# Performance work log

Hardware: AMD Instinct MI355X
Metric: run time of the kernel (lower is better)

The kernel has to match this reference:

```python
import math
import jax, jax.numpy as jnp
import numpy as np

N_HEAD = 16
N_CLUSTER = 64
GROUP_SIZE = 256


def _sinusoidal(n, d):
    # emb[p, 2j] = sin(p*div_j), emb[p, 2j+1] = cos(p*div_j)  (interleaved, as in torch source)
    pos = jnp.arange(n, dtype=jnp.float32)[:, None]
    div = jnp.exp(jnp.arange(0, d, 2, dtype=jnp.float32) * (-math.log(10000.0) / d))
    ang = pos * div  # [n, d//2]
    return jnp.stack([jnp.sin(ang), jnp.cos(ang)], axis=-1).reshape(n, d)


def _rotary(pe, x):
    # Faithful to source: sin = first half of interleaved table, cos = second half,
    # and the function RETURNS ONLY the rotated term (not x*cos + rot*sin).
    d = x.shape[-1]
    sin, cos = pe[..., : d // 2], pe[..., d // 2 :]
    x_even, x_odd = x[..., ::2], x[..., 1::2]
    out = jnp.stack([-x_odd * cos, x_even * sin], axis=-1)
    return out.reshape(jnp.broadcast_shapes(x.shape[:-1] + (d // 2,), out.shape[:-1]) + (2,)).reshape(x.shape) if False else jnp.broadcast_to(out, x.shape[:-1] + (d // 2, 2)).reshape(x.shape)


def _forward(x, w_attn, b_attn, w_proj, b_proj, w_assign):
    B, T, C = x.shape
    H, nc, gs = N_HEAD, N_CLUSTER, GROUP_SIZE
    hd = C // H
    ntpc = T // nc                 # tokens per cluster
    G = T // gs                    # number of groups
    ncpg = gs // ntpc              # clusters summarized per group
    c_max = (G - 1) * ncpg         # max cluster-KV length (padded)

    qkv = x @ w_attn.T + b_attn    # [B, T, 3C]
    q, k, v = jnp.split(qkv, 3, axis=-1)

    # ---- soft cluster summarization (block-diagonal softmax over each cluster's tokens) ----
    x_r = x.reshape(B, nc, ntpc, C)
    logits = jnp.einsum('bctd,cd->bct', x_r, w_assign)        # only diagonal cluster survives the mask
    w = jax.nn.softmax(logits, axis=-1)                        # [B, nc, ntpc]
    ck = jnp.einsum('bct,bctd->bcd', w, k.reshape(B, nc, ntpc, C))  # [B, nc, C]
    cv = jnp.einsum('bct,bctd->bcd', w, v.reshape(B, nc, ntpc, C))

    # ---- split into groups & heads ----
    qg = q.reshape(B, G, gs, H, hd).transpose(0, 1, 3, 2, 4)   # [B,G,H,gs,hd]
    kl = k.reshape(B, G, gs, H, hd).transpose(0, 1, 3, 2, 4)
    vl = v.reshape(B, G, gs, H, hd).transpose(0, 1, 3, 2, 4)
    kc = ck[:, :c_max].reshape(B, c_max, H, hd)                # [B,c_max,H,hd]
    vc = cv[:, :c_max].reshape(B, c_max, H, hd)

    # ---- rotary (positions restart per group; cluster tokens occupy positions 0..c-1) ----
    S = _sinusoidal(c_max + gs, hd)
    qr = _rotary(S[:gs], qg)                                   # q positions 0..gs-1 in every group
    kcr = _rotary(S[:c_max, None, :], kc)                      # cluster slot j -> position j
    pos_local = jnp.arange(G)[:, None] * ncpg + jnp.arange(gs)[None, :]  # [G,gs]
    klr = _rotary(S[pos_local][None, :, None], kl)             # local key p in group g -> pos g*ncpg+p

    # ---- attention: cluster KV (fully visible, masked to first g*ncpg) + local causal ----
    scale = 1.0 / math.sqrt(hd)
    sc = jnp.einsum('bghqd,bchd->bghqc', qr, kcr) * scale      # [B,G,H,gs,c_max]
    sl = jnp.einsum('bghqd,bghkd->bghqk', qr, klr) * scale     # [B,G,H,gs,gs]
    cmask = jnp.arange(c_max)[None, :] < (jnp.arange(G) * ncpg)[:, None]  # [G,c_max]
    sc = jnp.where(cmask[None, :, None, None, :], sc, -jnp.inf)
    lmask = jnp.tril(jnp.ones((gs, gs), dtype=bool))
    sl = jnp.where(lmask, sl, -jnp.inf)
    p = jax.nn.softmax(jnp.concatenate([sc, sl], axis=-1), axis=-1)
    pc, pl = p[..., :c_max], p[..., c_max:]
    y = jnp.einsum('bghqc,bchd->bghqd', pc, vc) + jnp.einsum('bghqk,bghkd->bghqd', pl, vl)
    y = y.transpose(0, 1, 3, 2, 4).reshape(B, T, C)
    return y @ w_proj.T + b_proj


def setup_inputs() -> dict:
    key = jax.random.key(0)
    ks = jax.random.split(key, 4)
    B, T, C, NC = 4, 4096, 1024, N_CLUSTER
    x = jax.random.normal(ks[0], (B, T, C), jnp.float32)
    w_attn = jax.random.normal(ks[1], (3 * C, C), jnp.float32) * 0.02
    b_attn = jnp.zeros((3 * C,), jnp.float32)
    w_proj = jax.random.normal(ks[2], (C, C), jnp.float32) * 0.02
    b_proj = jnp.zeros((C,), jnp.float32)
    w_assign = jax.random.normal(ks[3], (NC, C), jnp.float32) * 0.02
    return {"x": x, "w_attn": w_attn, "b_attn": b_attn, "w_proj": w_proj, "b_proj": b_proj, "w_assign": w_assign}


def reference(x, w_attn, b_attn, w_proj, b_proj, w_assign):
    return _forward(x, w_attn, b_attn, w_proj, b_proj, w_assign)
```

## Files before the change

### kernel.cpp

```cpp
#include <hip/hip_runtime.h>
#include <stdint.h>

typedef unsigned short u16;
typedef unsigned int   u32;
typedef __attribute__((ext_vector_type(8))) short short8;
typedef __attribute__((ext_vector_type(4))) short short4v;
typedef __attribute__((ext_vector_type(4))) float float4v;
typedef __attribute__((ext_vector_type(4))) u32   uint4v;

#define B_  4
#define T_  4096
#define C_  1024
#define H_  16
#define G_  16
#define GS_ 256
#define NC_ 64

static __device__ __forceinline__ u16 f2bf(float f){
  union{float f; u32 u;} c; c.f = f;
  return (u16)((c.u + 0x7fffu + ((c.u >> 16) & 1u)) >> 16);
}
static __device__ __forceinline__ float bf2f(u16 u){
  union{u32 u; float f;} c; c.u = ((u32)u) << 16; return c.f;
}
static __device__ __forceinline__ void gload16(const void* g, void* l){
  __builtin_amdgcn_global_load_lds((__attribute__((address_space(1))) void*)g,
                                   (__attribute__((address_space(3))) void*)l, 16, 0, 0);
}
static __device__ __forceinline__ short8 rot8(short8 v, const float* Sp, int i0){
  union{ short8 s; u32 u[4]; } a, o; a.s = v;
  #pragma unroll
  for(int p = 0; p < 4; p++){
    float e0 = bf2f((u16)(a.u[p] & 0xffffu));
    float e1 = bf2f((u16)(a.u[p] >> 16));
    float sn = Sp[i0 + p], cs = Sp[32 + i0 + p];
    o.u[p] = (u32)f2bf(-e1 * cs) | ((u32)f2bf(e0 * sn) << 16);
  }
  return o.s;
}

__global__ __launch_bounds__(256) void f2b_kernel(const float* __restrict__ s,
                                                  u16* __restrict__ d, int n4){
  int i = blockIdx.x * 256 + threadIdx.x;
  if(i >= n4) return;
  float4v v = *(const float4v*)(s + (size_t)i * 4);
  short4v o;
  o.x = (short)f2bf(v.x); o.y = (short)f2bf(v.y);
  o.z = (short)f2bf(v.z); o.w = (short)f2bf(v.w);
  *(short4v*)(d + (size_t)i * 4) = o;
}

__global__ void stab_kernel(float* __restrict__ S){
  int pos = blockIdx.x, d = threadIdx.x;
  int j = d >> 1;
  float div = expf((float)(2 * j) * (-0.14391156831212787f));
  float ang = (float)pos * div;
  S[pos * 64 + d] = (d & 1) ? cosf(ang) : sinf(ang);
}

template<int OUTBF>
__global__ __launch_bounds__(512, 1) void gemm8p(const u16* __restrict__ A,
    const u16* __restrict__ Bm, const float* __restrict__ bias,
    void* __restrict__ Cv, int M, int N, int K, int nbn)
{
  __shared__ u16 sA[2][2][256][32];
  __shared__ u16 sB[2][2][256][32];
  const int tid = threadIdx.x;
  const int lane = tid & 63, w = tid >> 6;
  const int l15 = lane & 15, l4 = lane >> 4;
  const int wr = w >> 2, wc = w & 3;

  const int cpx = gridDim.x >> 3;
  const int bid = blockIdx.x;
  const int swz = (bid & 7) * cpx + (bid >> 3);
  const int bm = swz / nbn, bn = swz - bm * nbn;
  const int row0 = bm * 256, col0 = bn * 256;

  float4v acc[8][4];
  #pragma unroll
  for(int m = 0; m < 8; m++)
    #pragma unroll
    for(int n = 0; n < 4; n++) acc[m][n] = (float4v){0.f, 0.f, 0.f, 0.f};

  const int srow = lane >> 2;
  const int sslot = lane & 3;

  auto stageHalf = [&](const u16* G, int grow0, u16* dstPlane, int ktOff){
    #pragma unroll
    for(int l = 0; l < 2; l++){
      int r = w * 32 + l * 16 + srow;
      int ss = sslot ^ ((r >> 1) & 3);
      gload16(G + (size_t)(grow0 + r) * K + ktOff + ss * 8,
              dstPlane + (w * 32 + l * 16) * 32);
    }
  };
  auto ldsReadA = [&](int d, int kk, int mh, short8* af){
    #pragma unroll
    for(int i = 0; i < 4; i++){
      int r = wr * 128 + (mh * 4 + i) * 16 + l15;
      int slot = l4 ^ ((r >> 1) & 3);
      af[i] = *(const short8*)&sA[d][kk][r][slot * 8];
    }
  };
  auto ldsReadB = [&](int d, int kk, short8* bf){
    #pragma unroll
    for(int i = 0; i < 4; i++){
      int r = wc * 64 + i * 16 + l15;
      int slot = l4 ^ ((r >> 1) & 3);
      bf[i] = *(const short8*)&sB[d][kk][r][slot * 8];
    }
  };
  auto mfma16 = [&](int mh, short8* af, short8* bf){
    __builtin_amdgcn_s_setprio(1);
    #pragma unroll
    for(int i = 0; i < 4; i++)
      #pragma unroll
      for(int n = 0; n < 4; n++)
        acc[mh * 4 + i][n] = __builtin_amdgcn_mfma_f32_16x16x32_bf16(af[i], bf[n], acc[mh * 4 + i][n], 0, 0, 0);
    __builtin_amdgcn_s_setprio(0);
  };

  stageHalf(A,  row0, &sA[0][0][0][0], 0);
  stageHalf(Bm, col0, &sB[0][0][0][0], 0);
  stageHalf(A,  row0, &sA[0][1][0][0], 32);
  stageHalf(Bm, col0, &sB[0][1][0][0], 32);
  asm volatile("s_waitcnt vmcnt(4)" ::: "memory");
  __builtin_amdgcn_s_barrier();

  const int nT = K >> 6;
  for(int t = 0; t < nT; t++){
    const int d = t & 1, dn = d ^ 1;
    const int ktN = (t + 1) << 6;
    const bool pf = (t + 1 < nT);
    short8 af[4], bf[4];

    ldsReadA(d, 0, 0, af); ldsReadB(d, 0, bf);
    if(pf) stageHalf(A, row0, &sA[dn][0][0][0], ktN);
    __builtin_amdgcn_s_barrier();
    mfma16(0, af, bf);
    __builtin_amdgcn_s_barrier();

    ldsReadA(d, 0, 1, af);
    if(pf) stageHalf(Bm, col0, &sB[dn][0][0][0], ktN);
    __builtin_amdgcn_s_barrier();
    mfma16(1, af, bf);
    if(pf) asm volatile("s_waitcnt vmcnt(4)" ::: "memory");
    else   asm volatile("s_waitcnt vmcnt(0)" ::: "memory");
    __builtin_amdgcn_s_barrier();

    ldsReadA(d, 1, 0, af); ldsReadB(d, 1, bf);
    if(pf) stageHalf(A, row0, &sA[dn][1][0][0], ktN + 32);
    __builtin_amdgcn_s_barrier();
    mfma16(0, af, bf);
    __builtin_amdgcn_s_barrier();

    ldsReadA(d, 1, 1, af);
    if(pf) stageHalf(Bm, col0, &sB[dn][1][0][0], ktN + 32);
    __builtin_amdgcn_s_barrier();
    mfma16(1, af, bf);
    if(pf) asm volatile("s_waitcnt vmcnt(4)" ::: "memory");
    __builtin_amdgcn_s_barrier();
  }

  #pragma unroll
  for(int m = 0; m < 8; m++){
    #pragma unroll
    for(int n = 0; n < 4; n++){
      int col = col0 + wc * 64 + n * 16 + l15;
      float bv = bias[col];
      #pragma unroll
      for(int j = 0; j < 4; j++){
        int row = row0 + wr * 128 + m * 16 + l4 * 4 + j;
        float v = acc[m][n][j] + bv;
        if(OUTBF) ((u16*)Cv)[(size_t)row * N + col] = f2bf(v);
        else      ((float*)Cv)[(size_t)row * N + col] = v;
      }
    }
  }
}

__global__ __launch_bounds__(256) void cluster_kernel(
    const float* __restrict__ x, const float* __restrict__ wasn,
    const u16* __restrict__ qkv, const float* __restrict__ S,
    u16* __restrict__ ckr, u16* __restrict__ vct)
{
  const int bc = blockIdx.x;
  const int c = bc & 63, b = bc >> 6;
  const int tid = threadIdx.x;
  const int lane = tid & 63, wv = tid >> 6;
  __shared__ float wgt[64];

  const float* xrow = x + ((size_t)b * T_ + c * 64) * C_;
  float4v wa4[4];
  #pragma unroll
  for(int ch = 0; ch < 4; ch++)
    wa4[ch] = *(const float4v*)(wasn + c * C_ + ch * 256 + lane * 4);

  for(int it = 0; it < 16; it++){
    int t = it * 4 + wv;
    const float* xr = xrow + (size_t)t * C_;
    float p = 0.f;
    #pragma unroll
    for(int ch = 0; ch < 4; ch++){
      float4v xv = *(const float4v*)(xr + ch * 256 + lane * 4);
      p += xv.x * wa4[ch].x + xv.y * wa4[ch].y + xv.z * wa4[ch].z + xv.w * wa4[ch].w;
    }
    p += __shfl_down(p, 32); p += __shfl_down(p, 16); p += __shfl_down(p, 8);
    p += __shfl_down(p, 4);  p += __shfl_down(p, 2);  p += __shfl_down(p, 1);
    if(lane == 0) wgt[t] = p;
  }
  __syncthreads();
  if(wv == 0){
    float v = wgt[lane];
    float mx = v;
    mx = fmaxf(mx, __shfl_xor(mx, 32)); mx = fmaxf(mx, __shfl_xor(mx, 16));
    mx = fmaxf(mx, __shfl_xor(mx, 8));  mx = fmaxf(mx, __shfl_xor(mx, 4));
    mx = fmaxf(mx, __shfl_xor(mx, 2));  mx = fmaxf(mx, __shfl_xor(mx, 1));
    float e = __expf(v - mx);
    float sm = e;
    sm += __shfl_xor(sm, 32); sm += __shfl_xor(sm, 16); sm += __shfl_xor(sm, 8);
    sm += __shfl_xor(sm, 4);  sm += __shfl_xor(sm, 2);  sm += __shfl_xor(sm, 1);
    wgt[lane] = e / sm;
  }
  __syncthreads();

  const int d0 = tid * 4;
  float ak[4] = {0, 0, 0, 0}, av[4] = {0, 0, 0, 0};
  const u16* krow = qkv + ((size_t)b * T_ + c * 64) * 3072 + C_ + d0;
  for(int t = 0; t < 64; t++){
    float wt = wgt[t];
    short4v kv = *(const short4v*)(krow + (size_t)t * 3072);
    short4v vv = *(const short4v*)(krow + (size_t)t * 3072 + C_);
    ak[0] += wt * bf2f((u16)kv.x); ak[1] += wt * bf2f((u16)kv.y);
    ak[2] += wt * bf2f((u16)kv.z); ak[3] += wt * bf2f((u16)kv.w);
    av[0] += wt * bf2f((u16)vv.x); av[1] += wt * bf2f((u16)vv.y);
    av[2] += wt * bf2f((u16)vv.z); av[3] += wt * bf2f((u16)vv.w);
  }
  const int dh = d0 & 63, i0 = dh >> 1;
  const float* Sp = S + c * 64;
  float s0 = Sp[i0],     c0 = Sp[32 + i0];
  float s1 = Sp[i0 + 1], c1 = Sp[32 + i0 + 1];
  short4v ck4;
  ck4.x = (short)f2bf(-ak[1] * c0); ck4.y = (short)f2bf(ak[0] * s0);
  ck4.z = (short)f2bf(-ak[3] * c1); ck4.w = (short)f2bf(ak[2] * s1);
  *(short4v*)(ckr + ((size_t)b * NC_ + c) * C_ + d0) = ck4;
  const int h = d0 >> 6;
  u16* vctb = vct + ((size_t)b * H_ + h) * 4096;
  #pragma unroll
  for(int i = 0; i < 4; i++){
    int d = dh + i;
    int col = ((c >> 2) ^ (d & 7)) * 4 + (c & 3);
    vctb[d * 64 + col] = f2bf(av[i]);
  }
}

__global__ __launch_bounds__(256) void vtrans_kernel(const u16* __restrict__ qkv,
                                                     u16* __restrict__ vt){
  const int bid = blockIdx.x;
  const int h = bid & 15, g = (bid >> 4) & 15, b = bid >> 8;
  const int tid = threadIdx.x;
  __shared__ u16 tile[256 * 80];
  const u16* src = qkv + ((size_t)b * T_ + g * GS_) * 3072 + 2 * C_ + h * 64;
  #pragma unroll
  for(int it = 0; it < 8; it++){
    int ch = it * 256 + tid;
    int k = ch >> 3, dd0 = (ch & 7) * 8;
    *(uint4v*)(tile + k * 80 + dd0) = *(const uint4v*)(src + (size_t)k * 3072 + dd0);
  }
  __syncthreads();
  u32* dst = (u32*)(vt + (size_t)bid * 64 * 256);
  #pragma unroll
  for(int it = 0; it < 32; it++){
    int u = it * 256 + tid;
    int d = u >> 7, kp = u & 127;
    int k = kp * 2;
    u32 a  = tile[k * 80 + d];
    u32 bb = tile[(k + 1) * 80 + d];
    int col2 = ((k >> 2) ^ (d & 7)) * 2 + (kp & 1);
    dst[d * 128 + col2] = a | (bb << 16);
  }
}

__global__ __launch_bounds__(512, 4) void attn4_kernel(
    const u16* __restrict__ qkv, const u16* __restrict__ ckr,
    const u16* __restrict__ vct, const u16* __restrict__ vt,
    const float* __restrict__ S, u16* __restrict__ y)
{
  const int bid = blockIdx.x;
  const int h = bid & 15, g = (bid >> 4) & 15, b = bid >> 8;
  const int tid = threadIdx.x;
  const int lane = tid & 63, wv = tid >> 6;
  const int l15 = lane & 15, l4 = lane >> 4;
  const int rows0 = wv, rows1 = 15 - wv;

  __shared__ u16 SH[36864];
  u16* Ksh = SH;
  u16* Vsh = SH + 16384;
  u16* Vcl = SH + 32768;

  const size_t tok0 = (size_t)b * T_ + (size_t)g * GS_;

  {
    const u16* vtt = vt + (((size_t)b * 16 + g) * 16 + h) * 16384;
    #pragma unroll
    for(int c = 0; c < 4; c++)
      gload16(vtt + (c * 512 + tid) * 8, Vsh + c * 4096 + wv * 512);
    gload16(vct + ((size_t)b * H_ + h) * 4096 + tid * 8, Vcl + wv * 512);
  }
  {
    const u16* kg = qkv + tok0 * 3072 + C_ + h * 64;
    #pragma unroll
    for(int c = 0; c < 4; c++){
      int idx = c * 512 + tid;
      int row = idx >> 3;
      int s0  = idx & 7;
      short8 v = *(const short8*)(kg + (size_t)row * 3072 + s0 * 8);
      short8 rv = rot8(v, S + (g * 4 + row) * 64, s0 * 4);
      *(short8*)(Ksh + row * 64 + (s0 ^ (row & 7)) * 8) = rv;
    }
  }
  short8 qa[2][2];
  #pragma unroll
  for(int f = 0; f < 2; f++){
    int rf = f ? rows1 : rows0;
    int qr = rf * 16 + l15;
    const u16* qp = qkv + (tok0 + qr) * 3072 + h * 64;
    #pragma unroll
    for(int kk = 0; kk < 2; kk++)
      qa[f][kk] = rot8(*(const short8*)(qp + kk * 32 + l4 * 8),
                       S + qr * 64, kk * 16 + l4 * 4);
  }
  __syncthreads();

  float4v o[2][4], osum[2];
  float mst[2];
  #pragma unroll
  for(int f = 0; f < 2; f++){
    osum[f] = (float4v){0, 0, 0, 0};
    mst[f] = -1e30f;
    #pragma unroll
    for(int n = 0; n < 4; n++) o[f][n] = (float4v){0, 0, 0, 0};
  }

  auto sm_update = [&](int f, float4v* st){
    float mx = st[0][0];
    #pragma unroll
    for(int n = 0; n < 4; n++)
      #pragma unroll
      for(int r = 0; r < 4; r++) mx = fmaxf(mx, st[n][r]);
    mx = fmaxf(mx, __shfl_xor(mx, 16));
    mx = fmaxf(mx, __shfl_xor(mx, 32));
    float mOld = mst[f];
    if(!__all(mx <= mOld)){
      float mn = fmaxf(mOld, mx);
      float rsc = __expf(mOld - mn);
      mst[f] = mn;
      float r0 = __shfl(rsc, l4 * 4 + 0);
      float r1 = __shfl(rsc, l4 * 4 + 1);
      float r2 = __shfl(rsc, l4 * 4 + 2);
      float r3 = __shfl(rsc, l4 * 4 + 3);
      #pragma unroll
      for(int n = 0; n < 4; n++){
        o[f][n][0] *= r0; o[f][n][1] *= r1; o[f][n][2] *= r2; o[f][n][3] *= r3;
      }
      osum[f][0] *= r0; osum[f][1] *= r1; osum[f][2] *= r2; osum[f][3] *= r3;
    }
    float mm = mst[f];
    #pragma unroll
    for(int n = 0; n < 4; n++)
      #pragma unroll
      for(int r = 0; r < 4; r++) st[n][r] = __expf(st[n][r] - mm);
  };

  auto pv = [&](int f, float4v* st, const u16* vb, int vstride, int granBase){
    #pragma unroll
    for(int kb = 0; kb < 4; kb++){
      union{ short8 s; u32 u[4]; } pa;
      pa.u[0] = (u32)f2bf(st[kb][0]) | ((u32)f2bf(st[kb][1]) << 16);
      pa.u[1] = (u32)f2bf(st[kb][2]) | ((u32)f2bf(st[kb][3]) << 16);
      pa.u[2] = 0; pa.u[3] = 0;
      union{ short8 s; u32 u[4]; } on;
      on.u[0] = 0x3F803F80u; on.u[1] = 0x3F803F80u; on.u[2] = 0; on.u[3] = 0;
      __builtin_amdgcn_s_setprio(1);
      osum[f] = __builtin_amdgcn_mfma_f32_16x16x32_bf16(pa.s, on.s, osum[f], 0, 0, 0);
      #pragma unroll
      for(int dn = 0; dn < 4; dn++){
        int d = dn * 16 + l15;
        int g2 = (granBase + kb * 4 + l4) ^ (l15 & 7);
        union{ short8 s; u32 u[4]; } vf;
        short4v v4 = *(const short4v*)(vb + d * vstride + g2 * 4);
        vf.u[0] = (u32)(u16)v4.x | ((u32)(u16)v4.y << 16);
        vf.u[1] = (u32)(u16)v4.z | ((u32)(u16)v4.w << 16);
        vf.u[2] = 0; vf.u[3] = 0;
        o[f][dn] = __builtin_amdgcn_mfma_f32_16x16x32_bf16(pa.s, vf.s, o[f][dn], 0, 0, 0);
      }
      __builtin_amdgcn_s_setprio(0);
    }
  };

  if(g > 0){
    const int climit = g * 4;
    #pragma unroll
    for(int f = 0; f < 2; f++){
      float4v st[4];
      #pragma unroll
      for(int n = 0; n < 4; n++) st[n] = (float4v){0, 0, 0, 0};
      #pragma unroll
      for(int kk = 0; kk < 2; kk++){
        __builtin_amdgcn_s_setprio(1);
        #pragma unroll
        for(int n = 0; n < 4; n++){
          short8 kf = *(const short8*)(ckr + ((size_t)b * NC_ + n * 16 + l15) * C_
                                       + h * 64 + kk * 32 + l4 * 8);
          st[n] = __builtin_amdgcn_mfma_f32_16x16x32_bf16(kf, qa[f][kk], st[n], 0, 0, 0);
        }
        __builtin_amdgcn_s_setprio(0);
      }
      #pragma unroll
      for(int n = 0; n < 4; n++)
        #pragma unroll
        for(int r = 0; r < 4; r++){
          int col = n * 16 + l4 * 4 + r;
          st[n][r] = (col >= climit) ? -1e30f : st[n][r] * 0.125f;
        }
      sm_update(f, st);
      pv(f, st, Vcl, 64, 0);
    }
  }

  const int ktA = rows0 >> 2, ktB = rows1 >> 2;
  for(int kt = 0; kt <= ktB; kt++){
    #pragma unroll
    for(int f = 0; f < 2; f++){
      int rf = f ? rows1 : rows0;
      if(kt > (f ? ktB : ktA)) continue;
      float4v st[4];
      #pragma unroll
      for(int n = 0; n < 4; n++) st[n] = (float4v){0, 0, 0, 0};
      #pragma unroll
      for(int kk = 0; kk < 2; kk++){
        __builtin_amdgcn_s_setprio(1);
        #pragma unroll
        for(int n = 0; n < 4; n++){
          int krow = kt * 64 + n * 16 + l15;
          int slot = (kk * 4 + l4) ^ (krow & 7);
          short8 kf = *(const short8*)(Ksh + krow * 64 + slot * 8);
          st[n] = __builtin_amdgcn_mfma_f32_16x16x32_bf16(kf, qa[f][kk], st[n], 0, 0, 0);
        }
        __builtin_amdgcn_s_setprio(0);
      }
      #pragma unroll
      for(int n = 0; n < 4; n++)
        #pragma unroll
        for(int r = 0; r < 4; r++){
          int col = kt * 64 + n * 16 + l4 * 4 + r;
          int q   = rf * 16 + l15;
          st[n][r] = (col > q) ? -1e30f : st[n][r] * 0.125f;
        }
      sm_update(f, st);
      pv(f, st, Vsh, 256, kt * 16);
    }
  }

  __syncthreads();
  u16* st_ = SH + wv * 2304;
  #pragma unroll
  for(int f = 0; f < 2; f++)
    #pragma unroll
    for(int r = 0; r < 4; r++){
      float inv = 1.0f / osum[f][r];
      #pragma unroll
      for(int n = 0; n < 4; n++)
        st_[(f * 16 + l4 * 4 + r) * 72 + n * 16 + l15] = f2bf(o[f][n][r] * inv);
    }
  #pragma unroll
  for(int f = 0; f < 2; f++){
    int rf = f ? rows1 : rows0;
    #pragma unroll
    for(int pass = 0; pass < 8; pass++){
      int rloc = pass * 2 + (lane >> 5);
      u32 val = *(const u32*)(st_ + (f * 16 + rloc) * 72 + (lane & 31) * 2);
      *(u32*)(y + (tok0 + rf * 16 + rloc) * C_ + h * 64 + (lane & 31) * 2) = val;
    }
  }
}

extern "C" void kernel_launch(void* const* d_in, const int* in_sizes, int n_in,
                              void* d_out, int out_size, void* d_ws, size_t ws_size,
                              hipStream_t stream)
{
  const float* x      = (const float*)d_in[0];
  const float* w_attn = (const float*)d_in[1];
  const float* b_attn = (const float*)d_in[2];
  const float* w_proj = (const float*)d_in[3];
  const float* b_proj = (const float*)d_in[4];
  const float* wasn   = (const float*)d_in[5];
  float* out = (float*)d_out;
  char* ws = (char*)d_ws;

  u16* qkv  = (u16*)(ws);
  u16* xb   = (u16*)(ws + 100663296);
  u16* vt   = (u16*)(ws + 134217728);
  u16* wab  = (u16*)(ws + 167772160);
  u16* wpb  = (u16*)(ws + 174063616);
  u16* ckr  = (u16*)(ws + 176160768);
  u16* vct  = (u16*)(ws + 176685056);
  float* st = (float*)(ws + 177209344);
  if(ws_size < 177290240) return;

  f2b_kernel<<<16384, 256, 0, stream>>>(x, xb, 4194304);
  f2b_kernel<<<3072, 256, 0, stream>>>(w_attn, wab, 786432);
  f2b_kernel<<<1024, 256, 0, stream>>>(w_proj, wpb, 262144);
  stab_kernel<<<316, 64, 0, stream>>>(st);
  gemm8p<1><<<768, 512, 0, stream>>>(xb, wab, b_attn, (void*)qkv, 16384, 3072, 1024, 12);
  cluster_kernel<<<256, 256, 0, stream>>>(x, wasn, qkv, st, ckr, vct);
  vtrans_kernel<<<1024, 256, 0, stream>>>(qkv, vt);
  attn4_kernel<<<1024, 512, 0, stream>>>(qkv, ckr, vct, vt, st, xb );
  gemm8p<0><<<256, 512, 0, stream>>>(xb, wpb, b_proj, (void*)out, 16384, 1024, 1024, 4);
}
```

Before: 285.1 us.

## Fuse V transpose into QKV GEMM epilogue and reuse its buffer for attention output

The QKV GEMM epilogue now writes the swizzled, transposed V tiles directly for the V column blocks, so the separate vtrans kernel launch and its extra pass over V are gone. The attention kernel writes its normalized output in place into the same per-(batch, group, head) V slot in token-major layout, dropping the LDS staging and barrier step. The output projection GEMM gets a new A-addressing mode that reads this head-blocked layout. The cost is extra scattered 32-bit stores in the QKV GEMM epilogue, and a reliance on each attention block finishing its reads of a slot before it overwrites that slot.

```diff
diff --git a/kernel.cpp b/kernel.cpp
--- a/kernel.cpp
+++ b/kernel.cpp
@@ -58,10 +58,10 @@
   S[pos * 64 + d] = (d & 1) ? cosf(ang) : sinf(ang);
 }
 
-template<int OUTBF>
+template<int MODE>
 __global__ __launch_bounds__(512, 1) void gemm8p(const u16* __restrict__ A,
     const u16* __restrict__ Bm, const float* __restrict__ bias,
-    void* __restrict__ Cv, int M, int N, int K, int nbn)
+    void* __restrict__ Cv, u16* __restrict__ vtout, int M, int N, int K, int nbn)
 {
   __shared__ u16 sA[2][2][256][32];
   __shared__ u16 sB[2][2][256][32];
@@ -85,12 +85,29 @@
   const int srow = lane >> 2;
   const int sslot = lane & 3;
 
-  auto stageHalf = [&](const u16* G, int grow0, u16* dstPlane, int ktOff){
+  auto stageHalfA = [&](u16* dstPlane, int ktOff){
     #pragma unroll
     for(int l = 0; l < 2; l++){
       int r = w * 32 + l * 16 + srow;
       int ss = sslot ^ ((r >> 1) & 3);
-      gload16(G + (size_t)(grow0 + r) * K + ktOff + ss * 8,
+      const u16* src;
+      if(MODE == 2){
+        int bg = (row0 + r) >> 8;
+        int hh = ktOff >> 6;
+        int coff = (ktOff & 63) + ss * 8;
+        src = A + ((size_t)(bg * 16 + hh)) * 16384 + (size_t)(r & 255) * 64 + coff;
+      } else {
+        src = A + (size_t)(row0 + r) * K + ktOff + ss * 8;
+      }
+      gload16(src, dstPlane + (w * 32 + l * 16) * 32);
+    }
+  };
+  auto stageHalfB = [&](u16* dstPlane, int ktOff){
+    #pragma unroll
+    for(int l = 0; l < 2; l++){
+      int r = w * 32 + l * 16 + srow;
+      int ss = sslot ^ ((r >> 1) & 3);
+      gload16(Bm + (size_t)(col0 + r) * K + ktOff + ss * 8,
               dstPlane + (w * 32 + l * 16) * 32);
     }
   };
@@ -120,10 +137,10 @@
     __builtin_amdgcn_s_setprio(0);
   };
 
-  stageHalf(A,  row0, &sA[0][0][0][0], 0);
-  stageHalf(Bm, col0, &sB[0][0][0][0], 0);
-  stageHalf(A,  row0, &sA[0][1][0][0], 32);
-  stageHalf(Bm, col0, &sB[0][1][0][0], 32);
+  stageHalfA(&sA[0][0][0][0], 0);
+  stageHalfB(&sB[0][0][0][0], 0);
+  stageHalfA(&sA[0][1][0][0], 32);
+  stageHalfB(&sB[0][1][0][0], 32);
   asm volatile("s_waitcnt vmcnt(4)" ::: "memory");
   __builtin_amdgcn_s_barrier();
 
@@ -135,13 +152,13 @@
     short8 af[4], bf[4];
 
     ldsReadA(d, 0, 0, af); ldsReadB(d, 0, bf);
-    if(pf) stageHalf(A, row0, &sA[dn][0][0][0], ktN);
+    if(pf) stageHalfA(&sA[dn][0][0][0], ktN);
     __builtin_amdgcn_s_barrier();
     mfma16(0, af, bf);
     __builtin_amdgcn_s_barrier();
 
     ldsReadA(d, 0, 1, af);
-    if(pf) stageHalf(Bm, col0, &sB[dn][0][0][0], ktN);
+    if(pf) stageHalfB(&sB[dn][0][0][0], ktN);
     __builtin_amdgcn_s_barrier();
     mfma16(1, af, bf);
     if(pf) asm volatile("s_waitcnt vmcnt(4)" ::: "memory");
@@ -149,13 +166,13 @@
     __builtin_amdgcn_s_barrier();
 
     ldsReadA(d, 1, 0, af); ldsReadB(d, 1, bf);
-    if(pf) stageHalf(A, row0, &sA[dn][1][0][0], ktN + 32);
+    if(pf) stageHalfA(&sA[dn][1][0][0], ktN + 32);
     __builtin_amdgcn_s_barrier();
     mfma16(0, af, bf);
     __builtin_amdgcn_s_barrier();
 
     ldsReadA(d, 1, 1, af);
-    if(pf) stageHalf(Bm, col0, &sB[dn][1][0][0], ktN + 32);
+    if(pf) stageHalfB(&sB[dn][1][0][0], ktN + 32);
     __builtin_amdgcn_s_barrier();
     mfma16(1, af, bf);
     if(pf) asm volatile("s_waitcnt vmcnt(4)" ::: "memory");
@@ -172,8 +189,27 @@
       for(int j = 0; j < 4; j++){
         int row = row0 + wr * 128 + m * 16 + l4 * 4 + j;
         float v = acc[m][n][j] + bv;
-        if(OUTBF) ((u16*)Cv)[(size_t)row * N + col] = f2bf(v);
-        else      ((float*)Cv)[(size_t)row * N + col] = v;
+        acc[m][n][j] = v;
+        if(MODE == 1) ((u16*)Cv)[(size_t)row * N + col] = f2bf(v);
+        else          ((float*)Cv)[(size_t)row * N + col] = v;
+      }
+    }
+  }
+  if(MODE == 1 && col0 >= 2048){
+    const int b = row0 >> 12, g = (row0 >> 8) & 15;
+    const int h = ((col0 - 2048) >> 6) + wc;
+    u32* vbase = (u32*)(vtout + (((size_t)(b * 16 + g)) * 16 + h) * 16384);
+    #pragma unroll
+    for(int n = 0; n < 4; n++){
+      int d = n * 16 + l15;
+      #pragma unroll
+      for(int m = 0; m < 8; m++){
+        int kb = (wr * 128 + m * 16 + l4 * 4) >> 2;
+        int col2 = (kb ^ (d & 7)) << 1;
+        u32 lo = (u32)f2bf(acc[m][n][0]) | ((u32)f2bf(acc[m][n][1]) << 16);
+        u32 hi = (u32)f2bf(acc[m][n][2]) | ((u32)f2bf(acc[m][n][3]) << 16);
+        vbase[d * 128 + col2]     = lo;
+        vbase[d * 128 + col2 + 1] = hi;
       }
     }
   }
@@ -254,37 +290,10 @@
   }
 }
 
-__global__ __launch_bounds__(256) void vtrans_kernel(const u16* __restrict__ qkv,
-                                                     u16* __restrict__ vt){
-  const int bid = blockIdx.x;
-  const int h = bid & 15, g = (bid >> 4) & 15, b = bid >> 8;
-  const int tid = threadIdx.x;
-  __shared__ u16 tile[256 * 80];
-  const u16* src = qkv + ((size_t)b * T_ + g * GS_) * 3072 + 2 * C_ + h * 64;
-  #pragma unroll
-  for(int it = 0; it < 8; it++){
-    int ch = it * 256 + tid;
-    int k = ch >> 3, dd0 = (ch & 7) * 8;
-    *(uint4v*)(tile + k * 80 + dd0) = *(const uint4v*)(src + (size_t)k * 3072 + dd0);
-  }
-  __syncthreads();
-  u32* dst = (u32*)(vt + (size_t)bid * 64 * 256);
-  #pragma unroll
-  for(int it = 0; it < 32; it++){
-    int u = it * 256 + tid;
-    int d = u >> 7, kp = u & 127;
-    int k = kp * 2;
-    u32 a  = tile[k * 80 + d];
-    u32 bb = tile[(k + 1) * 80 + d];
-    int col2 = ((k >> 2) ^ (d & 7)) * 2 + (kp & 1);
-    dst[d * 128 + col2] = a | (bb << 16);
-  }
-}
-
 __global__ __launch_bounds__(512, 4) void attn4_kernel(
     const u16* __restrict__ qkv, const u16* __restrict__ ckr,
-    const u16* __restrict__ vct, const u16* __restrict__ vt,
-    const float* __restrict__ S, u16* __restrict__ y)
+    const u16* __restrict__ vct, u16* __restrict__ vt,
+    const float* __restrict__ S)
 {
   const int bid = blockIdx.x;
   const int h = bid & 15, g = (bid >> 4) & 15, b = bid >> 8;
@@ -299,12 +308,12 @@
   u16* Vcl = SH + 32768;
 
   const size_t tok0 = (size_t)b * T_ + (size_t)g * GS_;
+  u16* vslot = vt + (((size_t)b * 16 + g) * 16 + h) * 16384;
 
   {
-    const u16* vtt = vt + (((size_t)b * 16 + g) * 16 + h) * 16384;
     #pragma unroll
     for(int c = 0; c < 4; c++)
-      gload16(vtt + (c * 512 + tid) * 8, Vsh + c * 4096 + wv * 512);
+      gload16(vslot + (c * 512 + tid) * 8, Vsh + c * 4096 + wv * 512);
     gload16(vct + ((size_t)b * H_ + h) * 4096 + tid * 8, Vcl + wv * 512);
   }
   {
@@ -462,25 +471,16 @@
     }
   }
 
-  __syncthreads();
-  u16* st_ = SH + wv * 2304;
-  #pragma unroll
-  for(int f = 0; f < 2; f++)
+  #pragma unroll
+  for(int f = 0; f < 2; f++){
+    int rf = f ? rows1 : rows0;
     #pragma unroll
     for(int r = 0; r < 4; r++){
       float inv = 1.0f / osum[f][r];
+      int kq = rf * 16 + l4 * 4 + r;
       #pragma unroll
       for(int n = 0; n < 4; n++)
-        st_[(f * 16 + l4 * 4 + r) * 72 + n * 16 + l15] = f2bf(o[f][n][r] * inv);
-    }
-  #pragma unroll
-  for(int f = 0; f < 2; f++){
-    int rf = f ? rows1 : rows0;
-    #pragma unroll
-    for(int pass = 0; pass < 8; pass++){
-      int rloc = pass * 2 + (lane >> 5);
-      u32 val = *(const u32*)(st_ + (f * 16 + rloc) * 72 + (lane & 31) * 2);
-      *(u32*)(y + (tok0 + rf * 16 + rloc) * C_ + h * 64 + (lane & 31) * 2) = val;
+        vslot[kq * 64 + n * 16 + l15] = f2bf(o[f][n][r] * inv);
     }
   }
 }
@@ -512,9 +512,8 @@
   f2b_kernel<<<3072, 256, 0, stream>>>(w_attn, wab, 786432);
   f2b_kernel<<<1024, 256, 0, stream>>>(w_proj, wpb, 262144);
   stab_kernel<<<316, 64, 0, stream>>>(st);
-  gemm8p<1><<<768, 512, 0, stream>>>(xb, wab, b_attn, (void*)qkv, 16384, 3072, 1024, 12);
+  gemm8p<1><<<768, 512, 0, stream>>>(xb, wab, b_attn, (void*)qkv, vt, 16384, 3072, 1024, 12);
   cluster_kernel<<<256, 256, 0, stream>>>(x, wasn, qkv, st, ckr, vct);
-  vtrans_kernel<<<1024, 256, 0, stream>>>(qkv, vt);
-  attn4_kernel<<<1024, 512, 0, stream>>>(qkv, ckr, vct, vt, st, xb );
-  gemm8p<0><<<256, 512, 0, stream>>>(xb, wpb, b_proj, (void*)out, 16384, 1024, 1024, 4);
-}
+  attn4_kernel<<<1024, 512, 0, stream>>>(qkv, ckr, vct, vt, st);
+  gemm8p<2><<<256, 512, 0, stream>>>(vt, wpb, b_proj, (void*)out, nullptr, 16384, 1024, 1024, 4);
+}
```

Result: faster. 271.4 us (-4.8%).
